# Kernel tuning notes

Hardware: AMD Instinct MI355X
Metric: run time of the kernel (lower is better)

The kernel has to match this reference:

```python
import jax, jax.numpy as jnp
import numpy as np

B, T, D, H, K = 128, 64, 2048, 512, 512
WINDOWS = [2, 3, 4]
ROUT = 2 * H            # bidirectional GRU output dim = 1024
FIN = ROUT + len(WINDOWS) * K + 2048 + 1024  # 5632 ('full' concat)
FOUT = 2048
BN_EPS = 1e-5


def setup_inputs() -> dict:
    key = jax.random.key(0)
    ks = jax.random.split(key, 32)
    s = 0.02
    inp = {
        "videos": jax.random.normal(ks[0], (B, T, D), jnp.float32),
        "motions": jax.random.normal(ks[1], (B, 1024), jnp.float32),
        "videos_origin": jax.random.normal(ks[2], (B, 2048), jnp.float32),
        "lengths": jax.random.randint(ks[3], (B,), 1, T + 1, jnp.int32),
        # GRU params (PyTorch layout: gates ordered r,z,n stacked on dim 0)
        "Wih_f": jax.random.normal(ks[4], (3 * H, D), jnp.float32) * s,
        "Whh_f": jax.random.normal(ks[5], (3 * H, H), jnp.float32) * s,
        "bih_f": jnp.zeros((3 * H,), jnp.float32),
        "bhh_f": jnp.zeros((3 * H,), jnp.float32),
        "Wih_b": jax.random.normal(ks[6], (3 * H, D), jnp.float32) * s,
        "Whh_b": jax.random.normal(ks[7], (3 * H, H), jnp.float32) * s,
        "bih_b": jnp.zeros((3 * H,), jnp.float32),
        "bhh_b": jnp.zeros((3 * H,), jnp.float32),
        # FC + BatchNorm1d (eval-mode) of MFC
        "fc_w": jax.random.normal(ks[8], (FOUT, FIN), jnp.float32) * (np.sqrt(6.0) / np.sqrt(FIN + FOUT)),
        "fc_b": jnp.zeros((FOUT,), jnp.float32),
        "bn_gamma": jnp.ones((FOUT,), jnp.float32),
        "bn_beta": jnp.zeros((FOUT,), jnp.float32),
        "bn_mean": jnp.zeros((FOUT,), jnp.float32),
        "bn_var": jnp.ones((FOUT,), jnp.float32),
    }
    for i, ws in enumerate(WINDOWS):
        inp[f"conv_w{ws}"] = jax.random.normal(ks[10 + 2 * i], (K, 1, ws, ROUT), jnp.float32) * s
        inp[f"conv_b{ws}"] = jnp.zeros((K,), jnp.float32)
    # mask consistent with lengths: mask[b,t] = t < lengths[b]
    inp["videos_mask"] = (jnp.arange(T)[None, :] < inp["lengths"][:, None]).astype(jnp.float32)
    return inp


def _gru_dir(x, Wih, Whh, bih, bhh, reverse):
    # x: [B,T,D] -> outputs [B,T,H]; torch GRU cell with r,z,n gate order
    xg = jnp.einsum("btd,gd->btg", x, Wih) + bih  # [B,T,3H] precomputed input gates

    def step(h, xg_t):
        hg = h @ Whh.T + bhh
        xr, xz, xn = jnp.split(xg_t, 3, axis=-1)
        hr, hz, hn = jnp.split(hg, 3, axis=-1)
        r = jax.nn.sigmoid(xr + hr)
        z = jax.nn.sigmoid(xz + hz)
        n = jnp.tanh(xn + r * hn)
        h_new = (1.0 - z) * n + z * h
        return h_new, h_new

    h0 = jnp.zeros((x.shape[0], Whh.shape[1]), x.dtype)
    _, hs = jax.lax.scan(step, h0, jnp.swapaxes(xg, 0, 1), reverse=reverse)
    return jnp.swapaxes(hs, 0, 1)


def _conv_branch(x4, w, b, ws):
    # x4: [B,1,T,ROUT], w: [K,1,ws,ROUT]; torch padding=(ws-1, 0)
    y = jax.lax.conv_general_dilated(
        x4, w, (1, 1), [(ws - 1, ws - 1), (0, 0)],
        dimension_numbers=("NCHW", "OIHW", "NCHW"))  # [B,K,T+ws-1,1]
    y = jax.nn.relu(y + b[None, :, None, None])
    return jnp.max(y, axis=(2, 3))  # max_pool1d over full time -> [B,K]


def _forward(videos, motions, videos_origin, lengths, videos_mask,
             Wih_f, Whh_f, bih_f, bhh_f, Wih_b, Whh_b, bih_b, bhh_b,
             conv_w2, conv_b2, conv_w3, conv_b3, conv_w4, conv_b4,
             fc_w, fc_b, bn_gamma, bn_beta, bn_mean, bn_var):
    fwd = _gru_dir(videos, Wih_f, Whh_f, bih_f, bhh_f, reverse=False)
    bwd = _gru_dir(videos, Wih_b, Whh_b, bih_b, bhh_b, reverse=True)
    gru_init_out = jnp.concatenate([fwd, bwd], axis=-1)  # [B,T,2H]

    # masked mean over valid frames (vectorized version of the batch for-loop)
    denom = lengths.astype(gru_init_out.dtype)[:, None]
    gru_out = jnp.sum(gru_init_out * videos_mask[:, :, None], axis=1) / denom  # [B,2H]

    masked = gru_init_out * videos_mask[:, :, None]
    x4 = masked[:, None, :, :]  # [B,1,T,2H]
    con_out = jnp.concatenate([
        _conv_branch(x4, conv_w2, conv_b2, 2),
        _conv_branch(x4, conv_w3, conv_b3, 3),
        _conv_branch(x4, conv_w4, conv_b4, 4),
    ], axis=1)  # [B,3K]

    # concate == 'full' (dropout is identity in eval)
    features = jnp.concatenate([gru_out, con_out, videos_origin, motions], axis=1)
    features = features @ fc_w.T + fc_b
    # BatchNorm1d, eval mode with running stats
    features = bn_gamma * (features - bn_mean) * jax.lax.rsqrt(bn_var + BN_EPS) + bn_beta
    # l2norm over dim 1
    features = features / jnp.sqrt(jnp.sum(features * features, axis=1, keepdims=True))
    return features


def reference(videos, motions, videos_origin, lengths, videos_mask,
              Wih_f, Whh_f, bih_f, bhh_f, Wih_b, Whh_b, bih_b, bhh_b,
              conv_w2, conv_b2, conv_w3, conv_b3, conv_w4, conv_b4,
              fc_w, fc_b, bn_gamma, bn_beta, bn_mean, bn_var):
    return _forward(videos, motions, videos_origin, lengths, videos_mask,
                    Wih_f, Whh_f, bih_f, bhh_f, Wih_b, Whh_b, bih_b, bhh_b,
                    conv_w2, conv_b2, conv_w3, conv_b3, conv_w4, conv_b4,
                    fc_w, fc_b, bn_gamma, bn_beta, bn_mean, bn_var)
```

## Files before the change

### kernel.cpp

```cpp
#include <hip/hip_runtime.h>
#include <hip/hip_bf16.h>
#include <stdint.h>

typedef __attribute__((ext_vector_type(8))) short short8;
typedef __attribute__((ext_vector_type(4))) float floatx4;
typedef __attribute__((ext_vector_type(4))) unsigned int u32x4;
typedef unsigned short u16;
typedef unsigned int u32;
typedef unsigned long long u64;

static __device__ __forceinline__ u16 f2bf(float f) {
  union { float f; u32 u; } v; v.f = f;
  return (u16)((v.u + 0x7fffu + ((v.u >> 16) & 1u)) >> 16);
}
static __device__ __forceinline__ float bf2f(u16 h) {
  union { u32 u; float f; } v; v.u = ((u32)h) << 16; return v.f;
}
static __device__ __forceinline__ u64 pack4(float a, float b, float c, float d) {
  return (u64)f2bf(a) | ((u64)f2bf(b) << 16) | ((u64)f2bf(c) << 32) | ((u64)f2bf(d) << 48);
}

__global__ __launch_bounds__(256) void k_fused_cvt(
    const float* __restrict__ videos, const float* __restrict__ Wih_f,
    const float* __restrict__ Wih_b, const float* __restrict__ Whh_f,
    const float* __restrict__ Whh_b, const float* __restrict__ fc_w,
    const float* __restrict__ w2, const float* __restrict__ w3,
    const float* __restrict__ w4, const float* __restrict__ vo,
    const float* __restrict__ mo, const float* __restrict__ bih_f,
    const float* __restrict__ bih_b, const float* __restrict__ fcb,
    const float* __restrict__ gam, const float* __restrict__ bet,
    const float* __restrict__ mu, const float* __restrict__ var,
    u16* __restrict__ vid, u16* __restrict__ wih, u16* __restrict__ whh,
    u16* __restrict__ fcw, u16* __restrict__ wc, u16* __restrict__ feat,
    float* __restrict__ bihcat, float* __restrict__ bns, float* __restrict__ bnt)
{
  const int O1 = 4194304;
  const int O2 = O1 + 786432;
  const int O3 = O2 + 786432;
  const int O4 = O3 + 196608;
  const int O5 = O4 + 196608;
  const int O6 = O5 + 2883584;
  const int O7 = O6 + 1179648;
  const int O8 = O7 + 65536;
  const int O9 = O8 + 32768;
  const int NQ = O9 + 1280;
  for (int q = blockIdx.x * 256 + threadIdx.x; q < NQ; q += gridDim.x * 256) {
    if (q < O1) {
      float4 v = ((const float4*)videos)[q];
      ((u64*)vid)[q] = pack4(v.x, v.y, v.z, v.w);
    } else if (q < O2) {
      int r = q - O1; float4 v = ((const float4*)Wih_f)[r];
      ((u64*)wih)[r] = pack4(v.x, v.y, v.z, v.w);
    } else if (q < O3) {
      int r = q - O2; float4 v = ((const float4*)Wih_b)[r];
      ((u64*)wih)[r + 786432] = pack4(v.x, v.y, v.z, v.w);
    } else if (q < O4) {
      int r = q - O3; float4 v = ((const float4*)Whh_f)[r];
      ((u64*)whh)[r] = pack4(v.x, v.y, v.z, v.w);
    } else if (q < O5) {
      int r = q - O4; float4 v = ((const float4*)Whh_b)[r];
      ((u64*)whh)[r + 196608] = pack4(v.x, v.y, v.z, v.w);
    } else if (q < O6) {
      int r = q - O5; float4 v = ((const float4*)fc_w)[r];
      ((u64*)fcw)[r] = pack4(v.x, v.y, v.z, v.w);
    } else if (q < O7) {
      int r = q - O6;
      int e = r << 2;
      int row = e >> 10, col = e & 1023;
      const float* src;
      if (row < 1024)      { int j = row >> 9, k = row & 511;                 src = w2 + (k * 2 + j) * 1024; }
      else if (row < 2560) { int m = row - 1024; int j = m >> 9, k = m & 511; src = w3 + (k * 3 + j) * 1024; }
      else                 { int m = row - 2560; int j = m >> 9, k = m & 511; src = w4 + (k * 4 + j) * 1024; }
      float4 v = *(const float4*)(src + col);
      ((u64*)wc)[r] = pack4(v.x, v.y, v.z, v.w);
    } else if (q < O8) {
      int r = q - O7; int b = r >> 9, c = (r & 511) * 4;
      float4 v = *(const float4*)&vo[(long)b * 2048 + c];
      *(u64*)&feat[(long)b * 5632 + 2560 + c] = pack4(v.x, v.y, v.z, v.w);
    } else if (q < O9) {
      int r = q - O8; int b = r >> 8, c = (r & 255) * 4;
      float4 v = *(const float4*)&mo[(long)b * 1024 + c];
      *(u64*)&feat[(long)b * 5632 + 4608 + c] = pack4(v.x, v.y, v.z, v.w);
    } else {
      int r = q - O9;
      if (r < 768) {
        int i = r * 4;
        const float* s = (i < 1536) ? (bih_f + i) : (bih_b + (i - 1536));
        *(float4*)&bihcat[i] = *(const float4*)s;
      } else {
        int i = (r - 768) * 4;
#pragma unroll
        for (int j = 0; j < 4; ++j) {
          int idx = i + j;
          float sc = gam[idx] * rsqrtf(var[idx] + 1e-5f);
          bns[idx] = sc;
          bnt[idx] = sc * (fcb[idx] - mu[idx]) + bet[idx];
        }
      }
    }
  }
}

static __device__ __forceinline__ void gload_lds16(const u16* g, u16* l) {
  __builtin_amdgcn_global_load_lds((const __attribute__((address_space(1))) u32*)(const void*)g,
                                   (__attribute__((address_space(3))) u32*)(void*)l, 16, 0, 0);
}

static __device__ __forceinline__ void stage_half_256(
    const u16* __restrict__ Mat, long K, int rowbase, int ktile, u16* lregion,
    int tid, int wid)
{
  int srow = tid >> 3;
  int sce = (((tid >> 3) ^ tid) & 7) * 8;
  const u16* g0 = Mat + (long)(rowbase + srow) * K + ktile * 64 + sce;
  const u16* g1 = Mat + (long)(rowbase + 64 + srow) * K + ktile * 64 + sce;
  gload_lds16(g0, lregion + wid * 512);
  gload_lds16(g1, lregion + 4096 + wid * 512);
}

__global__ __launch_bounds__(512) void gemm256(
    const u16* __restrict__ A, const u16* __restrict__ Bm,
    float* __restrict__ C, u16* __restrict__ C16, int M, int N, int K, int NT,
    const float* __restrict__ shift)
{
  __shared__ u16 lds[65536];
  int tid = threadIdx.x, lane = tid & 63, wid = tid >> 6;
  int r16 = lane & 15, kq = lane >> 4;
  int wr = wid >> 2, wc = wid & 3;
  int nwg = gridDim.x * gridDim.y;
  int lin = blockIdx.y * gridDim.x + blockIdx.x;
  int q8 = nwg >> 3;
  int swz = (lin & 7) * q8 + (lin >> 3);
  int m0 = (swz / gridDim.x) * 256, n0 = (swz % gridDim.x) * 256;

  int fxor = (r16 & 7) << 4;
  int c0 = (kq * 16) ^ fxor;
  int c1 = c0 ^ 64;
  int brow0 = (wc & 1) * 64;
  const char* ldsc = (const char*)lds;

  const floatx4 z4 = {0.f, 0.f, 0.f, 0.f};
  floatx4 acc[8][4];
#pragma unroll
  for (int i = 0; i < 8; ++i)
#pragma unroll
    for (int j = 0; j < 4; ++j) acc[i][j] = z4;

  stage_half_256(Bm, K, n0,       0, lds,                 tid, wid);
  stage_half_256(Bm, K, n0 + 128, 0, lds + 8192,          tid, wid);
  stage_half_256(A,  K, m0,       0, lds + 16384,         tid, wid);
  stage_half_256(A,  K, m0 + 128, 0, lds + 24576,         tid, wid);
  stage_half_256(Bm, K, n0,       1, lds + 32768,         tid, wid);
  stage_half_256(Bm, K, n0 + 128, 1, lds + 32768 + 8192,  tid, wid);
  stage_half_256(A,  K, m0,       1, lds + 32768 + 16384, tid, wid);
  stage_half_256(A,  K, m0 + 128, 1, lds + 32768 + 24576, tid, wid);
  asm volatile("s_waitcnt vmcnt(8)" ::: "memory");
  asm volatile("s_barrier" ::: "memory");

#define MFMA_CLUSTER(q)                                                        \
  asm volatile("s_waitcnt lgkmcnt(0)" ::: "memory");                           \
  __builtin_amdgcn_sched_barrier(0);                                           \
  __builtin_amdgcn_s_setprio(1);                                               \
  _Pragma("unroll")                                                            \
  for (int s = 0; s < 2; ++s)                                                  \
    _Pragma("unroll")                                                          \
    for (int e = 0; e < 2; ++e)                                                \
      _Pragma("unroll")                                                        \
      for (int j = 0; j < 4; ++j)                                              \
        acc[(q)*2 + e][j] = __builtin_amdgcn_mfma_f32_16x16x32_bf16(           \
            af[e][s], bf[j][s], acc[(q)*2 + e][j], 0, 0, 0);                   \
  __builtin_amdgcn_s_setprio(0);

  for (int T = 0; T < NT; ++T) {
    int P = T & 1;
    int Tn1 = (T + 1 < NT) ? T + 1 : 0;
    int Tn2 = (T + 2 < NT) ? T + 2 : T + 2 - NT;
    const char* bbase = ldsc + P * 65536 + (wc >> 1) * 16384;
    const char* abase = ldsc + P * 65536 + 32768 + wr * 16384;
    short8 bf[4][2];
    {
#pragma unroll
      for (int j = 0; j < 4; ++j) {
        bf[j][0] = *(const short8*)(bbase + (brow0 + j * 16 + r16) * 128 + c0);
        bf[j][1] = *(const short8*)(bbase + (brow0 + j * 16 + r16) * 128 + c1);
      }
      short8 af[2][2];
#pragma unroll
      for (int e = 0; e < 2; ++e) {
        af[e][0] = *(const short8*)(abase + (e * 16 + r16) * 128 + c0);
        af[e][1] = *(const short8*)(abase + (e * 16 + r16) * 128 + c1);
      }
      stage_half_256(A, K, m0, Tn1, lds + (Tn1 & 1) * 32768 + 16384, tid, wid);
      asm volatile("s_barrier" ::: "memory");
      MFMA_CLUSTER(0)
      asm volatile("s_barrier" ::: "memory");
    }
    {
      short8 af[2][2];
#pragma unroll
      for (int e = 0; e < 2; ++e) {
        af[e][0] = *(const short8*)(abase + ((2 + e) * 16 + r16) * 128 + c0);
        af[e][1] = *(const short8*)(abase + ((2 + e) * 16 + r16) * 128 + c1);
      }
      stage_half_256(A, K, m0 + 128, Tn1, lds + (Tn1 & 1) * 32768 + 24576, tid, wid);
      asm volatile("s_barrier" ::: "memory");
      MFMA_CLUSTER(1)
      asm volatile("s_barrier" ::: "memory");
    }
    {
      short8 af[2][2];
#pragma unroll
      for (int e = 0; e < 2; ++e) {
        af[e][0] = *(const short8*)(abase + ((4 + e) * 16 + r16) * 128 + c0);
        af[e][1] = *(const short8*)(abase + ((4 + e) * 16 + r16) * 128 + c1);
      }
      stage_half_256(Bm, K, n0, Tn2, lds + P * 32768, tid, wid);
      asm volatile("s_barrier" ::: "memory");
      MFMA_CLUSTER(2)
      asm volatile("s_barrier" ::: "memory");
    }
    {
      short8 af[2][2];
#pragma unroll
      for (int e = 0; e < 2; ++e) {
        af[e][0] = *(const short8*)(abase + ((6 + e) * 16 + r16) * 128 + c0);
        af[e][1] = *(const short8*)(abase + ((6 + e) * 16 + r16) * 128 + c1);
      }
      stage_half_256(Bm, K, n0 + 128, Tn2, lds + P * 32768 + 8192, tid, wid);
      asm volatile("s_barrier" ::: "memory");
      MFMA_CLUSTER(3)
      asm volatile("s_waitcnt vmcnt(4)" ::: "memory");
      asm volatile("s_barrier" ::: "memory");
    }
  }
#undef MFMA_CLUSTER

#pragma unroll
  for (int mf = 0; mf < 8; ++mf)
#pragma unroll
    for (int j = 0; j < 4; ++j) {
      int col = n0 + wc * 64 + j * 16 + r16;
      int row = m0 + wr * 128 + mf * 16 + kq * 4;
      if (C16) {
#pragma unroll
        for (int qq = 0; qq < 4; ++qq)
          C16[(long)(row + qq) * N + col] = f2bf(acc[mf][j][qq]);
      } else {
        float sh = shift ? shift[col] : 0.f;
#pragma unroll
        for (int qq = 0; qq < 4; ++qq)
          C[(long)(row + qq) * N + col] = acc[mf][j][qq] + sh;
      }
    }
}

__global__ __launch_bounds__(256) void gemm_bt(
    const u16* __restrict__ A, const u16* __restrict__ Bm,
    float* __restrict__ C, u16* __restrict__ C16, int M, int N, int K, int kn,
    const float* __restrict__ scale, const float* __restrict__ shift)
{
  __shared__ u16 As[128 * 32];
  __shared__ u16 Bs[128 * 32];
  int tid = threadIdx.x, lane = tid & 63, wid = tid >> 6;
  int nwg = gridDim.x * gridDim.y;
  int lin = blockIdx.y * gridDim.x + blockIdx.x;
  int q8 = nwg >> 3;
  int swz = (lin & 7) * q8 + (lin >> 3);
  int m0 = (swz / gridDim.x) * 128, n0 = (swz % gridDim.x) * 128;
  int kt0 = blockIdx.z * kn;
  int wr = wid >> 1, wc = wid & 1;
  int r16 = lane & 15, kq = lane >> 4;
  const floatx4 z4 = {0.f, 0.f, 0.f, 0.f};
  floatx4 acc[4][4];
#pragma unroll
  for (int i = 0; i < 4; ++i)
#pragma unroll
    for (int j = 0; j < 4; ++j) acc[i][j] = z4;
  for (int kt = kt0; kt < kt0 + kn; ++kt) {
    __syncthreads();
#pragma unroll
    for (int inst = 0; inst < 2; ++inst) {
      int g = inst * 256 + tid;
      int row = g >> 2, cb = g & 3;
      const u16* ga = A + (long)(m0 + row) * K + kt * 32 + cb * 8;
      const u16* gb = Bm + (long)(n0 + row) * K + kt * 32 + cb * 8;
      gload_lds16(ga, &As[(inst * 256 + wid * 64) * 8]);
      gload_lds16(gb, &Bs[(inst * 256 + wid * 64) * 8]);
    }
    __syncthreads();
    short8 af[4], bf[4];
#pragma unroll
    for (int mt = 0; mt < 4; ++mt) af[mt] = *(const short8*)&As[(wr * 64 + mt * 16 + r16) * 32 + kq * 8];
#pragma unroll
    for (int nt = 0; nt < 4; ++nt) bf[nt] = *(const short8*)&Bs[(wc * 64 + nt * 16 + r16) * 32 + kq * 8];
#pragma unroll
    for (int mt = 0; mt < 4; ++mt)
#pragma unroll
      for (int nt = 0; nt < 4; ++nt)
        acc[mt][nt] = __builtin_amdgcn_mfma_f32_16x16x32_bf16(af[mt], bf[nt], acc[mt][nt], 0, 0, 0);
  }
  float* Cp = C + (long)blockIdx.z * M * N;
#pragma unroll
  for (int nt = 0; nt < 4; ++nt) {
    int col = n0 + wc * 64 + nt * 16 + r16;
    float sc = scale ? scale[col] : 1.f;
    float sh = shift ? shift[col] : 0.f;
#pragma unroll
    for (int mt = 0; mt < 4; ++mt)
#pragma unroll
      for (int q = 0; q < 4; ++q) {
        int row = m0 + wr * 64 + mt * 16 + kq * 4 + q;
        float v = acc[mt][nt][q] * sc + sh;
        if (C16) C16[(long)row * N + col] = f2bf(v);
        else     Cp[(long)row * N + col] = v;
      }
  }
}

__global__ __launch_bounds__(512) void gru_rec(
    const float* __restrict__ xg,
    const u16* __restrict__ whhb,
    const float* __restrict__ bhh_f, const float* __restrict__ bhh_b,
    u16* __restrict__ hbuf,
    u16* __restrict__ maskb,
    u16* __restrict__ feat,
    const int* __restrict__ lengths,
    int* __restrict__ flg)
{
  __shared__ float part[2][4][3][256];
  __shared__ u16 hstage[8192];
  int tid = threadIdx.x, lane = tid & 63, wid = tid >> 6;
  int bid = blockIdx.x;
  int dir = bid >> 6, rem = bid & 63, bt = rem >> 3, is = rem & 7;
  int ih = wid & 3, ks = wid >> 2;
  int gbase = (dir * 8 + bt) * 32;
  int r16 = lane & 15, kq = lane >> 4;
  int iglob = is * 64 + ih * 16 + r16;
  int i0 = is * 64 + ih * 16 + kq * 4;
  int batch = bt * 16 + r16;
  int pollidx = (gbase + (lane & 31)) * 16;
  int pubidx = (gbase + is * 4 + ih) * 16;
  const float* bhh = dir ? bhh_b : bhh_f;
  const floatx4 z4 = {0.f, 0.f, 0.f, 0.f};
  int len = lengths[batch];

  short8 wfrag[3][8];
#pragma unroll
  for (int g = 0; g < 3; ++g) {
    const u16* wrow = whhb + (long)(dir * 1536 + g * 512 + iglob) * 512;
#pragma unroll
    for (int kk = 0; kk < 8; ++kk)
      wfrag[g][kk] = *(const short8*)&wrow[(ks * 8 + kk) * 32 + kq * 8];
  }
  float4 bh4[3];
#pragma unroll
  for (int g = 0; g < 3; ++g) bh4[g] = *(const float4*)&bhh[g * 512 + i0];
  float4 hprev = {0.f, 0.f, 0.f, 0.f};
  float4 msum = {0.f, 0.f, 0.f, 0.f};

  float4 px[3];
  if (ks == 0) {
    int ts0 = dir ? 63 : 0;
    long xb = (long)(batch * 64 + ts0) * 3072 + dir * 1536 + i0;
#pragma unroll
    for (int g = 0; g < 3; ++g) px[g] = *(const float4*)&xg[xb + g * 512];
  }

  int so0 = wid * 2048 + lane * 16;
  int so1 = so0 + 1024;
  char* sl0 = (char*)hstage + (so0 ^ (((so0 >> 10) & 7) << 4));
  char* sl1 = (char*)hstage + (so1 ^ (((so1 >> 10) & 7) << 4));
  int rb = r16 * 1024 + ks * 512 + kq * 16;
  int rsw = (r16 & 7) << 4;

  for (int t = 0; t < 64; ++t) {
    if (t > 0) {
      if (wid == 0) {
        while (true) {
          int v;
          asm volatile("global_load_dword %0, %1, off sc0 sc1\n\ts_waitcnt vmcnt(0)"
                       : "=v"(v) : "v"(&flg[pollidx]) : "memory");
          if (__all(v >= t)) break;
          __builtin_amdgcn_s_sleep(1);
        }
      }
      asm volatile("s_barrier" ::: "memory");
    }
    int par = t & 1;
    const char* hsrc = (const char*)(hbuf + (long)((par * 2 + dir) * 128 + bt * 16) * 512);
    u32x4 qa, qb;
    asm volatile(
      "global_load_dwordx4 %0, %2, off sc0 sc1\n\t"
      "global_load_dwordx4 %1, %3, off sc0 sc1"
      : "=&v"(qa), "=&v"(qb)
      : "v"(hsrc + so0), "v"(hsrc + so1)
      : "memory");
    asm volatile("s_waitcnt vmcnt(0)" ::: "memory");
    *(u32x4*)sl0 = qa;
    *(u32x4*)sl1 = qb;
    float4 pxn[3];
    if (ks == 0 && t < 63) {
      int ts1 = dir ? (62 - t) : (t + 1);
      long xb = (long)(batch * 64 + ts1) * 3072 + dir * 1536 + i0;
#pragma unroll
      for (int g = 0; g < 3; ++g) pxn[g] = *(const float4*)&xg[xb + g * 512];
    }
    asm volatile("s_waitcnt lgkmcnt(0)\n\ts_barrier" ::: "memory");
    floatx4 acc[3];
#pragma unroll
    for (int g = 0; g < 3; ++g) acc[g] = z4;
#pragma unroll
    for (int kk = 0; kk < 8; ++kk) {
      short8 hv = *(const short8*)((const char*)hstage + ((rb + kk * 64) ^ rsw));
#pragma unroll
      for (int g = 0; g < 3; ++g)
        acc[g] = __builtin_amdgcn_mfma_f32_16x16x32_bf16(wfrag[g][kk], hv, acc[g], 0, 0, 0);
    }
    if (ks == 1) {
#pragma unroll
      for (int g = 0; g < 3; ++g) *(floatx4*)&part[par][ih][g][lane * 4] = acc[g];
    }
    asm volatile("s_waitcnt lgkmcnt(0)\n\ts_barrier" ::: "memory");
    if (ks == 0) {
      int tsrc = dir ? (63 - t) : t;
#pragma unroll
      for (int g = 0; g < 3; ++g) acc[g] += *(const floatx4*)&part[par][ih][g][lane * 4];
      float4 hn4;
#pragma unroll
      for (int q = 0; q < 4; ++q) {
        float rr = acc[0][q] + ((const float*)&bh4[0])[q] + ((const float*)&px[0])[q];
        float zz = acc[1][q] + ((const float*)&bh4[1])[q] + ((const float*)&px[1])[q];
        float r = 1.f / (1.f + __expf(-rr));
        float z = 1.f / (1.f + __expf(-zz));
        float n = tanhf(((const float*)&px[2])[q] + r * (acc[2][q] + ((const float*)&bh4[2])[q]));
        ((float*)&hn4)[q] = (1.f - z) * n + z * ((const float*)&hprev)[q];
      }
      hprev = hn4;
      u16* hdst = hbuf + (long)(((par ^ 1) * 2 + dir) * 128 + bt * 16) * 512;
      u64 hval = pack4(hn4.x, hn4.y, hn4.z, hn4.w);
      asm volatile("global_store_dwordx2 %0, %1, off sc0 sc1"
                   :: "v"((u64*)&hdst[r16 * 512 + i0]), "v"(hval) : "memory");
      if (t < 63) {
        asm volatile("s_waitcnt vmcnt(0)" ::: "memory");
        if (lane == 0) {
          int tv = t + 1;
          asm volatile("global_store_dword %0, %1, off sc0 sc1"
                       :: "v"(&flg[pubidx]), "v"(tv) : "memory");
        }
      }
      bool mv = tsrc < len;
      *(u64*)&maskb[(long)(batch * 64 + tsrc) * 1024 + dir * 512 + i0] = mv ? hval : 0ull;
      if (mv) {
        msum.x += hn4.x; msum.y += hn4.y; msum.z += hn4.z; msum.w += hn4.w;
      }
      px[0] = pxn[0]; px[1] = pxn[1]; px[2] = pxn[2];
    }
  }
  if (ks == 0) {
    float inv = 1.0f / (float)len;
    *(u64*)&feat[(long)batch * 5632 + dir * 512 + i0] =
        pack4(msum.x * inv, msum.y * inv, msum.z * inv, msum.w * inv);
  }
}

__global__ __launch_bounds__(256) void k_conv_finish(
    const u16* __restrict__ z, const float* __restrict__ cb2,
    const float* __restrict__ cb3, const float* __restrict__ cb4,
    u16* __restrict__ feat)
{
  int b = blockIdx.x, wsi = blockIdx.y, k2 = threadIdx.x * 2;
  int ws = wsi + 2;
  int base = (wsi == 0) ? 0 : (wsi == 1 ? 1024 : 2560);
  const float* cb = (wsi == 0) ? cb2 : (wsi == 1 ? cb3 : cb4);
  float bias0 = cb[k2], bias1 = cb[k2 + 1];
  float m0 = 0.f, m1 = 0.f;
  for (int p = 0; p < 64 + ws - 1; ++p) {
    float a0 = bias0, a1 = bias1;
    for (int j = 0; j < ws; ++j) {
      int t = p - (ws - 1) + j;
      if (t >= 0 && t < 64) {
        u32 v = *(const u32*)&z[(long)(b * 64 + t) * 4608 + base + j * 512 + k2];
        a0 += bf2f((u16)v);
        a1 += bf2f((u16)(v >> 16));
      }
    }
    m0 = fmaxf(m0, a0);
    m1 = fmaxf(m1, a1);
  }
  *(u32*)&feat[(long)b * 5632 + 1024 + wsi * 512 + k2] = (u32)f2bf(m0) | ((u32)f2bf(m1) << 16);
}

__global__ __launch_bounds__(256) void k_l2norm(const float* __restrict__ p,
    const float* __restrict__ bns, const float* __restrict__ bnt, float* __restrict__ out)
{
  __shared__ float red[4];
  int b = blockIdx.x, tid = threadIdx.x;
  float v[8]; float s = 0.f;
#pragma unroll
  for (int j = 0; j < 8; ++j) {
    int i = j * 256 + tid;
    long o = (long)b * 2048 + i;
    float a = 0.f;
#pragma unroll
    for (int zz = 0; zz < 8; ++zz) a += p[o + (long)zz * 262144];
    a = a * bns[i] + bnt[i];
    v[j] = a; s += a * a;
  }
#pragma unroll
  for (int o = 32; o > 0; o >>= 1) s += __shfl_down(s, o);
  if ((tid & 63) == 0) red[tid >> 6] = s;
  __syncthreads();
  float rn = rsqrtf(red[0] + red[1] + red[2] + red[3]);
#pragma unroll
  for (int j = 0; j < 8; ++j)
    out[(long)b * 2048 + j * 256 + tid] = v[j] * rn;
}

extern "C" void kernel_launch(void* const* d_in, const int* in_sizes, int n_in,
                              void* d_out, int out_size, void* d_ws, size_t ws_size,
                              hipStream_t stream)
{
  (void)in_sizes; (void)n_in; (void)out_size; (void)ws_size;
  const float* videos       = (const float*)d_in[0];
  const float* motions      = (const float*)d_in[1];
  const float* videos_origin= (const float*)d_in[2];
  const int*   lengths      = (const int*)d_in[3];
  const float* Wih_f = (const float*)d_in[4];
  const float* Whh_f = (const float*)d_in[5];
  const float* bih_f = (const float*)d_in[6];
  const float* bhh_f = (const float*)d_in[7];
  const float* Wih_b = (const float*)d_in[8];
  const float* Whh_b = (const float*)d_in[9];
  const float* bih_b = (const float*)d_in[10];
  const float* bhh_b = (const float*)d_in[11];
  const float* fc_w  = (const float*)d_in[12];
  const float* fc_b  = (const float*)d_in[13];
  const float* bn_gamma = (const float*)d_in[14];
  const float* bn_beta  = (const float*)d_in[15];
  const float* bn_mean  = (const float*)d_in[16];
  const float* bn_var   = (const float*)d_in[17];
  const float* conv_w2 = (const float*)d_in[18];
  const float* conv_b2 = (const float*)d_in[19];
  const float* conv_w3 = (const float*)d_in[20];
  const float* conv_b3 = (const float*)d_in[21];
  const float* conv_w4 = (const float*)d_in[22];
  const float* conv_b4 = (const float*)d_in[23];
  float* out = (float*)d_out;
  char* w = (char*)d_ws;

  const size_t XG    = 0;
  const size_t VID   = 134217728;
  const size_t MASKB = 167772160;
  const size_t WIH   = 184549376;
  const size_t WHH   = 197132288;
  const size_t WC    = 200278016;
  const size_t FCW   = 209715200;
  const size_t FEAT  = 232783872;
  const size_t BIH   = 235274240;
  const size_t BNS   = 235286528;
  const size_t BNT   = 235294720;
  const size_t HB    = 235302912;
  const size_t FLG   = HB + 524288;

  float* xg   = (float*)(w + XG);
  u16*   zb16 = (u16*)(w + XG);
  u16* vid    = (u16*)(w + VID);
  u16* maskb  = (u16*)(w + MASKB);
  float* fcp  = (float*)(w + MASKB);
  u16* wih    = (u16*)(w + WIH);
  u16* whh    = (u16*)(w + WHH);
  u16* wc_    = (u16*)(w + WC);
  u16* fcw    = (u16*)(w + FCW);
  u16* feat   = (u16*)(w + FEAT);
  float* bih  = (float*)(w + BIH);
  float* bns  = (float*)(w + BNS);
  float* bnt  = (float*)(w + BNT);
  u16* hb     = (u16*)(w + HB);
  int* flg    = (int*)(w + FLG);

  hipMemsetAsync(w + HB, 0, 524288 + 32768, stream);

  k_fused_cvt<<<4096, 256, 0, stream>>>(
      videos, Wih_f, Wih_b, Whh_f, Whh_b, fc_w, conv_w2, conv_w3, conv_w4,
      videos_origin, motions, bih_f, bih_b, fc_b, bn_gamma, bn_beta, bn_mean, bn_var,
      vid, wih, whh, fcw, wc_, feat, bih, bns, bnt);

  gemm256<<<dim3(12, 32), 512, 0, stream>>>(vid, wih, xg, nullptr, 8192, 3072, 2048, 32, bih);

  {
    const float* xg_c = xg; const u16* whh_c = whh;
    u16* hb_c = hb; u16* mb_c = maskb; u16* ft_c = feat;
    const int* len_c = lengths; int* flg_c = flg;
    const float* bf_c = bhh_f; const float* bb_c = bhh_b;
    void* args[] = { (void*)&xg_c, (void*)&whh_c, (void*)&bf_c, (void*)&bb_c,
                     (void*)&hb_c, (void*)&mb_c, (void*)&ft_c, (void*)&len_c, (void*)&flg_c };
    hipLaunchCooperativeKernel(reinterpret_cast<void*>(gru_rec), dim3(128), dim3(512), args, 0, stream);
  }

  gemm256<<<dim3(18, 32), 512, 0, stream>>>(maskb, wc_, nullptr, zb16, 8192, 4608, 1024, 16, nullptr);
  k_conv_finish<<<dim3(128, 3), 256, 0, stream>>>(zb16, conv_b2, conv_b3, conv_b4, feat);
  gemm_bt<<<dim3(16, 1, 8), 256, 0, stream>>>(feat, fcw, fcp, nullptr, 128, 2048, 5632, 22, nullptr, nullptr);
  k_l2norm<<<128, 256, 0, stream>>>(fcp, bns, bnt, out);
}
```

Before: 608.7 us.

## Overlap later-stage weight conversions with GRU recurrence using extra cooperative blocks

Moves the fc_w, conv weight and feature-concat bf16 conversions out of the upfront conversion kernel and into 128 extra blocks of the cooperative GRU recurrence launch. The recurrence uses only 128 blocks and is latency-bound, so idle CUs can do this memory-bound work concurrently. The flag array stride is also compacted from 16 ints to 1 per entry, shrinking the memset. Packed flags may now share cache lines, which could change polling contention, and the extra blocks must co-reside for the cooperative launch.

```diff
diff --git a/kernel.cpp b/kernel.cpp
--- a/kernel.cpp
+++ b/kernel.cpp
@@ -20,18 +20,14 @@
   return (u64)f2bf(a) | ((u64)f2bf(b) << 16) | ((u64)f2bf(c) << 32) | ((u64)f2bf(d) << 48);
 }
 
-__global__ __launch_bounds__(256) void k_fused_cvt(
+__global__ __launch_bounds__(256) void k_pre_cvt(
     const float* __restrict__ videos, const float* __restrict__ Wih_f,
     const float* __restrict__ Wih_b, const float* __restrict__ Whh_f,
-    const float* __restrict__ Whh_b, const float* __restrict__ fc_w,
-    const float* __restrict__ w2, const float* __restrict__ w3,
-    const float* __restrict__ w4, const float* __restrict__ vo,
-    const float* __restrict__ mo, const float* __restrict__ bih_f,
+    const float* __restrict__ Whh_b, const float* __restrict__ bih_f,
     const float* __restrict__ bih_b, const float* __restrict__ fcb,
     const float* __restrict__ gam, const float* __restrict__ bet,
     const float* __restrict__ mu, const float* __restrict__ var,
     u16* __restrict__ vid, u16* __restrict__ wih, u16* __restrict__ whh,
-    u16* __restrict__ fcw, u16* __restrict__ wc, u16* __restrict__ feat,
     float* __restrict__ bihcat, float* __restrict__ bns, float* __restrict__ bnt)
 {
   const int O1 = 4194304;
@@ -39,11 +35,7 @@
   const int O3 = O2 + 786432;
   const int O4 = O3 + 196608;
   const int O5 = O4 + 196608;
-  const int O6 = O5 + 2883584;
-  const int O7 = O6 + 1179648;
-  const int O8 = O7 + 65536;
-  const int O9 = O8 + 32768;
-  const int NQ = O9 + 1280;
+  const int NQ = O5 + 1280;
   for (int q = blockIdx.x * 256 + threadIdx.x; q < NQ; q += gridDim.x * 256) {
     if (q < O1) {
       float4 v = ((const float4*)videos)[q];
@@ -60,29 +52,8 @@
     } else if (q < O5) {
       int r = q - O4; float4 v = ((const float4*)Whh_b)[r];
       ((u64*)whh)[r + 196608] = pack4(v.x, v.y, v.z, v.w);
-    } else if (q < O6) {
-      int r = q - O5; float4 v = ((const float4*)fc_w)[r];
-      ((u64*)fcw)[r] = pack4(v.x, v.y, v.z, v.w);
-    } else if (q < O7) {
-      int r = q - O6;
-      int e = r << 2;
-      int row = e >> 10, col = e & 1023;
-      const float* src;
-      if (row < 1024)      { int j = row >> 9, k = row & 511;                 src = w2 + (k * 2 + j) * 1024; }
-      else if (row < 2560) { int m = row - 1024; int j = m >> 9, k = m & 511; src = w3 + (k * 3 + j) * 1024; }
-      else                 { int m = row - 2560; int j = m >> 9, k = m & 511; src = w4 + (k * 4 + j) * 1024; }
-      float4 v = *(const float4*)(src + col);
-      ((u64*)wc)[r] = pack4(v.x, v.y, v.z, v.w);
-    } else if (q < O8) {
-      int r = q - O7; int b = r >> 9, c = (r & 511) * 4;
-      float4 v = *(const float4*)&vo[(long)b * 2048 + c];
-      *(u64*)&feat[(long)b * 5632 + 2560 + c] = pack4(v.x, v.y, v.z, v.w);
-    } else if (q < O9) {
-      int r = q - O8; int b = r >> 8, c = (r & 255) * 4;
-      float4 v = *(const float4*)&mo[(long)b * 1024 + c];
-      *(u64*)&feat[(long)b * 5632 + 4608 + c] = pack4(v.x, v.y, v.z, v.w);
     } else {
-      int r = q - O9;
+      int r = q - O5;
       if (r < 768) {
         int i = r * 4;
         const float* s = (i < 1536) ? (bih_f + i) : (bih_b + (i - 1536));
@@ -325,12 +296,50 @@
     u16* __restrict__ maskb,
     u16* __restrict__ feat,
     const int* __restrict__ lengths,
-    int* __restrict__ flg)
+    int* __restrict__ flg,
+    const float* __restrict__ fc_w, const float* __restrict__ w2,
+    const float* __restrict__ w3, const float* __restrict__ w4,
+    const float* __restrict__ vo, const float* __restrict__ mo,
+    u16* __restrict__ fcw, u16* __restrict__ wc)
 {
   __shared__ float part[2][4][3][256];
   __shared__ u16 hstage[8192];
   int tid = threadIdx.x, lane = tid & 63, wid = tid >> 6;
   int bid = blockIdx.x;
+
+  if (bid >= 128) {
+    int cid = bid - 128;
+    const int C1 = 2883584;
+    const int C2 = C1 + 1179648;
+    const int C3 = C2 + 65536;
+    const int NQ = C3 + 32768;
+    for (int q = cid * 512 + tid; q < NQ; q += 128 * 512) {
+      if (q < C1) {
+        float4 v = ((const float4*)fc_w)[q];
+        ((u64*)fcw)[q] = pack4(v.x, v.y, v.z, v.w);
+      } else if (q < C2) {
+        int r = q - C1;
+        int e = r << 2;
+        int row = e >> 10, col = e & 1023;
+        const float* src;
+        if (row < 1024)      { int j = row >> 9, k = row & 511;                 src = w2 + (k * 2 + j) * 1024; }
+        else if (row < 2560) { int m = row - 1024; int j = m >> 9, k = m & 511; src = w3 + (k * 3 + j) * 1024; }
+        else                 { int m = row - 2560; int j = m >> 9, k = m & 511; src = w4 + (k * 4 + j) * 1024; }
+        float4 v = *(const float4*)(src + col);
+        ((u64*)wc)[r] = pack4(v.x, v.y, v.z, v.w);
+      } else if (q < C3) {
+        int r = q - C2; int b = r >> 9, c = (r & 511) * 4;
+        float4 v = *(const float4*)&vo[(long)b * 2048 + c];
+        *(u64*)&feat[(long)b * 5632 + 2560 + c] = pack4(v.x, v.y, v.z, v.w);
+      } else {
+        int r = q - C3; int b = r >> 8, c = (r & 255) * 4;
+        float4 v = *(const float4*)&mo[(long)b * 1024 + c];
+        *(u64*)&feat[(long)b * 5632 + 4608 + c] = pack4(v.x, v.y, v.z, v.w);
+      }
+    }
+    return;
+  }
+
   int dir = bid >> 6, rem = bid & 63, bt = rem >> 3, is = rem & 7;
   int ih = wid & 3, ks = wid >> 2;
   int gbase = (dir * 8 + bt) * 32;
@@ -338,8 +347,8 @@
   int iglob = is * 64 + ih * 16 + r16;
   int i0 = is * 64 + ih * 16 + kq * 4;
   int batch = bt * 16 + r16;
-  int pollidx = (gbase + (lane & 31)) * 16;
-  int pubidx = (gbase + is * 4 + ih) * 16;
+  int pollidx = gbase + (lane & 31);
+  int pubidx = gbase + is * 4 + ih;
   const float* bhh = dir ? bhh_b : bhh_f;
   const floatx4 z4 = {0.f, 0.f, 0.f, 0.f};
   int len = lengths[batch];
@@ -578,12 +587,12 @@
   u16* hb     = (u16*)(w + HB);
   int* flg    = (int*)(w + FLG);
 
-  hipMemsetAsync(w + HB, 0, 524288 + 32768, stream);
-
-  k_fused_cvt<<<4096, 256, 0, stream>>>(
-      videos, Wih_f, Wih_b, Whh_f, Whh_b, fc_w, conv_w2, conv_w3, conv_w4,
-      videos_origin, motions, bih_f, bih_b, fc_b, bn_gamma, bn_beta, bn_mean, bn_var,
-      vid, wih, whh, fcw, wc_, feat, bih, bns, bnt);
+  hipMemsetAsync(w + HB, 0, 524288 + 2048, stream);
+
+  k_pre_cvt<<<4096, 256, 0, stream>>>(
+      videos, Wih_f, Wih_b, Whh_f, Whh_b, bih_f, bih_b,
+      fc_b, bn_gamma, bn_beta, bn_mean, bn_var,
+      vid, wih, whh, bih, bns, bnt);
 
   gemm256<<<dim3(12, 32), 512, 0, stream>>>(vid, wih, xg, nullptr, 8192, 3072, 2048, 32, bih);
 
@@ -592,9 +601,15 @@
     u16* hb_c = hb; u16* mb_c = maskb; u16* ft_c = feat;
     const int* len_c = lengths; int* flg_c = flg;
     const float* bf_c = bhh_f; const float* bb_c = bhh_b;
+    const float* fw_c = fc_w; const float* w2_c = conv_w2;
+    const float* w3_c = conv_w3; const float* w4_c = conv_w4;
+    const float* vo_c = videos_origin; const float* mo_c = motions;
+    u16* fcw_c = fcw; u16* wc_c = wc_;
     void* args[] = { (void*)&xg_c, (void*)&whh_c, (void*)&bf_c, (void*)&bb_c,
-                     (void*)&hb_c, (void*)&mb_c, (void*)&ft_c, (void*)&len_c, (void*)&flg_c };
-    hipLaunchCooperativeKernel(reinterpret_cast<void*>(gru_rec), dim3(128), dim3(512), args, 0, stream);
+                     (void*)&hb_c, (void*)&mb_c, (void*)&ft_c, (void*)&len_c, (void*)&flg_c,
+                     (void*)&fw_c, (void*)&w2_c, (void*)&w3_c, (void*)&w4_c,
+                     (void*)&vo_c, (void*)&mo_c, (void*)&fcw_c, (void*)&wc_c };
+    hipLaunchCooperativeKernel(reinterpret_cast<void*>(gru_rec), dim3(256), dim3(512), args, 0, stream);
   }
 
   gemm256<<<dim3(18, 32), 512, 0, stream>>>(maskb, wc_, nullptr, zb16, 8192, 4608, 1024, 16, nullptr);
```

New measurement: 594.0 us. 2.4% less time.
